# Optimization experiments

Hardware: AMD Instinct MI355X
Metric: run time of the kernel (lower is better)

## Reference

```python
import jax, jax.numpy as jnp
import numpy as np


def setup_inputs() -> dict:
    N, E, D = 50000, 800000, 64
    key = jax.random.key(0)
    ks = jax.random.split(key, 8)
    s = 1.0 / np.sqrt(2 * D)
    inp = {
        "node_emb": jax.random.normal(ks[0], (N, D), dtype=jnp.float32),
        "edge_index": jax.random.randint(ks[1], (2, E), 0, N, dtype=jnp.int64),
        "W1": jax.random.normal(ks[2], (2 * D, D), dtype=jnp.float32) * s,
        "b1": jnp.zeros((D,), dtype=jnp.float32),
        "W2": jax.random.normal(ks[3], (D, D), dtype=jnp.float32) * (1.0 / np.sqrt(D)),
        "b2": jnp.zeros((D,), dtype=jnp.float32),
        "Wg": jax.random.normal(ks[4], (D, D), dtype=jnp.float32) * (1.0 / np.sqrt(D)),
        "bg": jnp.zeros((D,), dtype=jnp.float32),
    }
    return inp


def reference(node_emb, edge_index, W1, b1, W2, b2, Wg, bg):
    # Gather pairwise embeddings along edges
    src, dst = edge_index[0], edge_index[1]
    pair_emb = jnp.concatenate([node_emb[src], node_emb[dst]], axis=-1)  # [E, 2D]
    # Interaction MLP (dropout in eval mode -> identity)
    h = jax.nn.relu(pair_emb @ W1 + b1)
    interaction = h @ W2 + b2  # [E, D]
    # Sigmoid gate
    gate = jax.nn.sigmoid(interaction @ Wg + bg)
    gated = interaction * gate  # [E, D]
    # Scatter-mean back to source nodes
    N = node_emb.shape[0]
    summed = jax.ops.segment_sum(gated, src, num_segments=N)  # [N, D]
    counts = jax.ops.segment_sum(jnp.ones((src.shape[0],), dtype=gated.dtype), src, num_segments=N)
    pooled = summed / jnp.maximum(counts, 1.0)[:, None]
    return pooled
```

## Files before the change

### kernel.cpp

```cpp
#include <hip/hip_runtime.h>


typedef unsigned short ushort_t;
typedef __attribute__((ext_vector_type(8))) short     bf16x8;
typedef __attribute__((ext_vector_type(8))) unsigned short u16x8;
typedef __attribute__((ext_vector_type(4))) float     f32x4;

constexpr int D        = 64;
constexpr int TILE     = 64;
constexpr int BLOCK    = 256;
constexpr int NFRAG    = 32;
constexpr int SLAB_B   = 4352;
constexpr int PAIR_STR = 136;
constexpr int H_STR    = 72;
constexpr float LOG2E  = 1.4426950408889634f;

static __device__ __forceinline__ ushort_t f2bf(float f) {
    union { float f; unsigned int u; } v; v.f = f;
    const unsigned int r = v.u + 0x7FFFu + ((v.u >> 16) & 1u);
    return (ushort_t)(r >> 16);
}

#if __has_builtin(__builtin_amdgcn_exp2f)
static __device__ __forceinline__ float fexp2(float x) { return __builtin_amdgcn_exp2f(x); }
#else
static __device__ __forceinline__ float fexp2(float x) {
    float r; asm("v_exp_f32 %0, %1" : "=v"(r) : "v"(x)); return r;
}
#endif
#if __has_builtin(__builtin_amdgcn_rcpf)
static __device__ __forceinline__ float frcp(float x) { return __builtin_amdgcn_rcpf(x); }
#else
static __device__ __forceinline__ float frcp(float x) {
    float r; asm("v_rcp_f32 %0, %1" : "=v"(r) : "v"(x)); return r;
}
#endif


__global__ void prep_kernel(const float* __restrict__ W1, const float* __restrict__ W2,
                            const float* __restrict__ Wg,
                            const float* __restrict__ b2, const float* __restrict__ bg,
                            const float* __restrict__ emb, const int* __restrict__ ei,
                            ushort_t* __restrict__ wpack, float* __restrict__ bgp,
                            ushort_t* __restrict__ emb_bf, int* __restrict__ cnt,
                            float* __restrict__ summed,
                            int total_emb, int cvt_blocks, int e4blocks, int E) {
    const int bid = blockIdx.x;
    if (bid < 64) {
        const int t = bid * 256 + threadIdx.x;
        const int f = t >> 9;
        const int l = (t >> 3) & 63;
        const int j = t & 7;
        const int k = ((f < 16) ? (f & 3) : ((f - 16) & 1)) * 32 + (l >> 4) * 8 + j;
        const int n = ((f < 16) ? (f >> 2) : (((f & 7)) >> 1)) * 16 + (l & 15);
        float v;
        if (f < 16)      v = W1[k * 64 + n];
        else if (f < 24) v = W2[k * 64 + n];
        else {
            float s = 0.f;
            const float* wr = W2 + k * 64;
#pragma unroll 8
            for (int m = 0; m < 64; ++m) s += wr[m] * Wg[m * 64 + n];
            v = s * LOG2E;
        }
        wpack[t] = f2bf(v);
    } else if (bid < 64 + cvt_blocks) {
        const int idx  = (bid - 64) * 256 + threadIdx.x;
        const int base = idx * 8;
        if (base < total_emb) {
            const float4 a = *(const float4*)(emb + base);
            const float4 b = *(const float4*)(emb + base + 4);
            u16x8 p;
            p[0]=f2bf(a.x); p[1]=f2bf(a.y); p[2]=f2bf(a.z); p[3]=f2bf(a.w);
            p[4]=f2bf(b.x); p[5]=f2bf(b.y); p[6]=f2bf(b.z); p[7]=f2bf(b.w);
            *(u16x8*)(emb_bf + base) = p;
        }
    } else if (bid == 64 + cvt_blocks) {
        const int n = threadIdx.x;
        if (n < 64) {
            float s = bg[n];
#pragma unroll 8
            for (int m = 0; m < 64; ++m) s += b2[m] * Wg[m * 64 + n];
            bgp[n] = s * LOG2E;
        }
    } else if (bid < 65 + cvt_blocks + e4blocks) {
        const int e = ((bid - 65 - cvt_blocks) * 256 + threadIdx.x) * 4;
        if (e + 3 < E) {
            const int4 v = *(const int4*)(ei + e);
            atomicAdd(&cnt[v.x], 1); atomicAdd(&cnt[v.y], 1);
            atomicAdd(&cnt[v.z], 1); atomicAdd(&cnt[v.w], 1);
        } else {
            for (int k = e; k < E; ++k) atomicAdd(&cnt[ei[k]], 1);
        }
    } else {
        const int idx  = (bid - 65 - cvt_blocks - e4blocks) * 256 + threadIdx.x;
        const int base = idx * 4;
        if (base < total_emb)
            *(float4*)(summed + base) = (float4){0.f, 0.f, 0.f, 0.f};
    }
}


__global__ void scan_block(const int* __restrict__ cnt, int* __restrict__ off,
                           int* __restrict__ bsum, int N) {
    __shared__ int s[256];
    const int t = threadIdx.x, i = blockIdx.x * 256 + t;
    const int x = (i < N) ? cnt[i] : 0;
    s[t] = x; __syncthreads();
    for (int d = 1; d < 256; d <<= 1) {
        const int v = (t >= d) ? s[t - d] : 0;
        __syncthreads();
        s[t] += v;
        __syncthreads();
    }
    if (i < N) off[i] = s[t] - x;
    if (t == 255) bsum[blockIdx.x] = s[255];
}

__global__ void scatter_idx(const int* __restrict__ ei, int* __restrict__ off,
                            const int* __restrict__ bsum, unsigned* __restrict__ sorted,
                            int E, int nb) {
    __shared__ int pref[256];
    const int t = threadIdx.x;
    const int x = (t < nb) ? bsum[t] : 0;
    pref[t] = x; __syncthreads();
    for (int d = 1; d < 256; d <<= 1) {
        const int v = (t >= d) ? pref[t - d] : 0;
        __syncthreads();
        pref[t] += v;
        __syncthreads();
    }
    const int e = (blockIdx.x * blockDim.x + t) * 4;
    if (e + 3 < E) {
        const int4 v = *(const int4*)(ei + e);
        const int4 d = *(const int4*)(ei + E + e);
        const int bx = v.x >> 8, by = v.y >> 8, bz = v.z >> 8, bw = v.w >> 8;
        sorted[(bx ? pref[bx - 1] : 0) + atomicAdd(&off[v.x], 1)] =
            ((unsigned)v.x << 16) | (unsigned)d.x;
        sorted[(by ? pref[by - 1] : 0) + atomicAdd(&off[v.y], 1)] =
            ((unsigned)v.y << 16) | (unsigned)d.y;
        sorted[(bz ? pref[bz - 1] : 0) + atomicAdd(&off[v.z], 1)] =
            ((unsigned)v.z << 16) | (unsigned)d.z;
        sorted[(bw ? pref[bw - 1] : 0) + atomicAdd(&off[v.w], 1)] =
            ((unsigned)v.w << 16) | (unsigned)d.w;
    } else {
        for (int k = e; k < E; ++k) {
            const int s = ei[k], b = s >> 8;
            sorted[(b ? pref[b - 1] : 0) + atomicAdd(&off[s], 1)] =
                ((unsigned)s << 16) | (unsigned)ei[E + k];
        }
    }
}


__global__ __launch_bounds__(BLOCK, 8)
void edge_mlp_mfma(const ushort_t* __restrict__ emb_bf,
                   const unsigned* __restrict__ sorted,
                   const ushort_t* __restrict__ wpack,
                   const float* __restrict__ b1, const float* __restrict__ b2,
                   const float* __restrict__ bgp,
                   const int*   __restrict__ cnt,
                   float* __restrict__ summed,
                   int E)
{
    __shared__ char  slab[4][SLAB_B];
    __shared__ int   srcIds[TILE];
    __shared__ float rcS[TILE];

    const int tid = threadIdx.x;

    {
        const int e = tid >> 2, q4 = tid & 3;
        ushort_t* prow = (ushort_t*)&slab[e >> 4][(e & 15) * (PAIR_STR * 2)];
        const int ide = blockIdx.x * TILE + e;
        if (ide < E) {
            const unsigned p = sorted[ide];
            const int s  = (int)(p >> 16);
            const int dn = (int)(p & 0xFFFFu);
            if (q4 == 0) { srcIds[e] = s; rcS[e] = frcp(fmaxf((float)cnt[s], 1.0f)); }
            const ushort_t* sr = emb_bf + (size_t)s  * D + q4 * 16;
            const ushort_t* dr = emb_bf + (size_t)dn * D + q4 * 16;
            *(u16x8*)&prow[q4 * 16]          = *(const u16x8*)sr;
            *(u16x8*)&prow[q4 * 16 + 8]      = *(const u16x8*)(sr + 8);
            *(u16x8*)&prow[64 + q4 * 16]     = *(const u16x8*)dr;
            *(u16x8*)&prow[64 + q4 * 16 + 8] = *(const u16x8*)(dr + 8);
        } else {
            if (q4 == 0) { srcIds[e] = -1; rcS[e] = 1.0f; }
            const u16x8 z = {0,0,0,0,0,0,0,0};
            *(u16x8*)&prow[q4 * 16]          = z;
            *(u16x8*)&prow[q4 * 16 + 8]      = z;
            *(u16x8*)&prow[64 + q4 * 16]     = z;
            *(u16x8*)&prow[64 + q4 * 16 + 8] = z;
        }
    }

    const int w    = tid >> 6;
    const int ln   = tid & 63;
    const int quad = ln >> 4;
    const int cn   = ln & 15;
    ushort_t* pairW = (ushort_t*)slab[w];
    ushort_t* hW    = (ushort_t*)slab[w];

    f32x4 acc1[4];
#pragma unroll
    for (int nt = 0; nt < 4; ++nt) {
        const float b = b1[nt * 16 + cn];
        acc1[nt] = (f32x4){b, b, b, b};
    }
#pragma unroll
    for (int kc = 0; kc < 4; ++kc) {
        const bf16x8 a = *(const bf16x8*)&pairW[cn * PAIR_STR + kc * 32 + quad * 8];
#pragma unroll
        for (int nt = 0; nt < 4; ++nt) {
            const bf16x8 bf = *(const bf16x8*)(wpack + ((nt * 4 + kc) * 64 + ln) * 8);
            acc1[nt] = __builtin_amdgcn_mfma_f32_16x16x32_bf16(a, bf, acc1[nt], 0, 0, 0);
        }
    }
#pragma unroll
    for (int nt = 0; nt < 4; ++nt)
#pragma unroll
        for (int r = 0; r < 4; ++r)
            hW[(quad * 4 + r) * H_STR + nt * 16 + cn] = f2bf(fmaxf(acc1[nt][r], 0.f));

    f32x4 acc2[4], accg[4];
#pragma unroll
    for (int nt = 0; nt < 4; ++nt) {
        const float b  = b2 [nt * 16 + cn];
        const float bG = bgp[nt * 16 + cn];
        acc2[nt] = (f32x4){b, b, b, b};
        accg[nt] = (f32x4){bG, bG, bG, bG};
    }
#pragma unroll
    for (int kc = 0; kc < 2; ++kc) {
        const bf16x8 a = *(const bf16x8*)&hW[cn * H_STR + kc * 32 + quad * 8];
#pragma unroll
        for (int nt = 0; nt < 4; ++nt) {
            const bf16x8 bf2 = *(const bf16x8*)(wpack + ((16 + nt * 2 + kc) * 64 + ln) * 8);
            const bf16x8 bfg = *(const bf16x8*)(wpack + ((24 + nt * 2 + kc) * 64 + ln) * 8);
            acc2[nt] = __builtin_amdgcn_mfma_f32_16x16x32_bf16(a, bf2, acc2[nt], 0, 0, 0);
            accg[nt] = __builtin_amdgcn_mfma_f32_16x16x32_bf16(a, bfg, accg[nt], 0, 0, 0);
        }
    }

    float P[4][4];
#pragma unroll
    for (int nt = 0; nt < 4; ++nt) {
#pragma unroll
        for (int r = 0; r < 4; ++r) {
            const float ex = fexp2(-accg[nt][r]);
            P[nt][r] = acc2[nt][r] * frcp(1.0f + ex);
        }
        P[nt][1] += P[nt][0];
        P[nt][2] += P[nt][1];
        P[nt][3] += P[nt][2];
    }

    {
        const int   rbase  = 16 * w;
        const int   myRow  = ln & 15;
        const int   mySrc  = srcIds[rbase + myRow];
        const float myRc   = rcS[rbase + myRow];
        const int   prevSrc = srcIds[rbase + ((myRow + 15) & 15)];
        unsigned bmask = ((unsigned)__ballot(mySrc != prevSrc) & 0xFFFFu) | 1u;
        const int q4r = 4 * quad;
        while (bmask) {
            const int a = __builtin_ctz(bmask);
            bmask &= (bmask - 1u);
            const int b = bmask ? __builtin_ctz(bmask) : 16;
            const int sseg = __builtin_amdgcn_readlane(mySrc, a);
            if (sseg >= 0) {
                const int lo  = a - q4r, hi = b - q4r;
                const int clo = lo < 0 ? 0 : (lo > 4 ? 4 : lo);
                const int chi = hi < 0 ? 0 : (hi > 4 ? 4 : hi);
                const bool ge1 = chi > 1, ge2 = chi > 2, ge3 = chi > 3;
                const bool l0 = clo > 0, l1 = clo > 1, l2 = clo > 2;
                const bool valid = chi > clo;
                float t[4];
#pragma unroll
                for (int nt = 0; nt < 4; ++nt) {
                    const float sh = ge2 ? (ge3 ? P[nt][3] : P[nt][2])
                                         : (ge1 ? P[nt][1] : P[nt][0]);
                    const float sl = l1 ? (l2 ? P[nt][2] : P[nt][1])
                                        : (l0 ? P[nt][0] : 0.f);
                    t[nt] = valid ? sh - sl : 0.f;
                }
                t[0] += __shfl_xor(t[0], 16); t[0] += __shfl_xor(t[0], 32);
                t[1] += __shfl_xor(t[1], 16); t[1] += __shfl_xor(t[1], 32);
                t[2] += __shfl_xor(t[2], 16); t[2] += __shfl_xor(t[2], 32);
                t[3] += __shfl_xor(t[3], 16); t[3] += __shfl_xor(t[3], 32);
                const float tot = (quad < 2) ? (quad == 0 ? t[0] : t[1])
                                             : (quad == 2 ? t[2] : t[3]);
                const float rc = __uint_as_float(
                    __builtin_amdgcn_readlane(__float_as_uint(myRc), a));
                unsafeAtomicAdd(&summed[(size_t)sseg * D + ln], tot * rc);
            }
        }
    }
}

extern "C" void kernel_launch(void* const* d_in, const int* in_sizes, int n_in,
                              void* d_out, int out_size, void* d_ws, size_t ws_size,
                              hipStream_t stream) {
    const float* node_emb   = (const float*)d_in[0];
    const int*   edge_index = (const int*)d_in[1];
    const float* W1 = (const float*)d_in[2];
    const float* b1 = (const float*)d_in[3];
    const float* W2 = (const float*)d_in[4];
    const float* b2 = (const float*)d_in[5];
    const float* Wg = (const float*)d_in[6];
    const float* bg = (const float*)d_in[7];

    const int N = in_sizes[0] / D;
    const int E = in_sizes[1] / 2;
    const int total_emb = N * D;

    int* cnt    = (int*)d_ws;
    int* off    = cnt + N;
    int* bsum   = off + N;
    unsigned* sorted = (unsigned*)(bsum + 256);
    float* bgp  = (float*)(sorted + E);
    ushort_t* wpack  = (ushort_t*)(bgp + 64);
    ushort_t* emb_bf = wpack + NFRAG * 512;

    float* summed = (float*)d_out;

    hipMemsetAsync(cnt, 0, sizeof(int) * (size_t)N, stream);

    const int cvt_blocks = (total_emb / 8 + 255) / 256;
    const int e4blocks   = ((E + 3) / 4 + 255) / 256;
    const int zblocks    = (total_emb / 4 + 255) / 256;
    prep_kernel<<<64 + cvt_blocks + 1 + e4blocks + zblocks, 256, 0, stream>>>(
        W1, W2, Wg, b2, bg, node_emb, edge_index,
        wpack, bgp, emb_bf, cnt, summed, total_emb, cvt_blocks, e4blocks, E);

    const int nblocks = (N + 255) / 256;
    scan_block <<<nblocks, 256, 0, stream>>>(cnt, off, bsum, N);
    scatter_idx<<<e4blocks, 256, 0, stream>>>(edge_index, off, bsum, sorted, E, nblocks);

    const int ntiles = (E + TILE - 1) / TILE;
    edge_mlp_mfma<<<ntiles, BLOCK, 0, stream>>>(emb_bf, sorted, wpack,
                                                b1, b2, bgp, cnt, summed, E);
}
```

Baseline: 237.5 us.

## Fuse preprocessing, count, scan and scatter into one cooperative kernel

Replaces the memset plus three preprocessing launches (prep, block scan, scatter) with a single cooperative persistent kernel that separates the phases with grid-wide syncs. Each block redoes the small block-sum scan locally in shared memory before scattering. The aim is to remove kernel launch gaps and the memset. The cost is a grid-stride loop over virtual blocks at limited occupancy, plus the overhead of the grid barriers. If the cooperative launch fails, it falls back to the old launches.

```diff
diff --git a/kernel.cpp b/kernel.cpp
--- a/kernel.cpp
+++ b/kernel.cpp
@@ -1,5 +1,8 @@
 #include <hip/hip_runtime.h>
-
+#include <hip/hip_cooperative_groups.h>
+
+
+namespace cg = cooperative_groups;
 
 typedef unsigned short ushort_t;
 typedef __attribute__((ext_vector_type(8))) short     bf16x8;
@@ -35,6 +38,133 @@
     float r; asm("v_rcp_f32 %0, %1" : "=v"(r) : "v"(x)); return r;
 }
 #endif
+
+
+struct AuxParams {
+    const float* W1; const float* W2; const float* Wg;
+    const float* b2; const float* bg;
+    const float* emb; const int* ei;
+    ushort_t* wpack; float* bgp; ushort_t* emb_bf;
+    int* cnt; int* off; int* bsum; unsigned* sorted; float* summed;
+    int N, E, total_emb, cvt_blocks, e4blocks, zblocks, nblocks;
+};
+
+__global__ __launch_bounds__(BLOCK, 8)
+void fused_aux(AuxParams P) {
+    cg::grid_group grid = cg::this_grid();
+    __shared__ int s[256];
+    const int tid = threadIdx.x;
+    const int G   = gridDim.x;
+
+    for (int i = blockIdx.x * BLOCK + tid; i < P.N; i += G * BLOCK) P.cnt[i] = 0;
+    grid.sync();
+
+    const int vb1 = 65 + P.cvt_blocks + P.e4blocks + P.zblocks;
+    for (int vb = blockIdx.x; vb < vb1; vb += G) {
+        if (vb < 64) {
+            const int t = vb * 256 + tid;
+            const int f = t >> 9;
+            const int l = (t >> 3) & 63;
+            const int j = t & 7;
+            const int k = ((f < 16) ? (f & 3) : ((f - 16) & 1)) * 32 + (l >> 4) * 8 + j;
+            const int n = ((f < 16) ? (f >> 2) : (((f & 7)) >> 1)) * 16 + (l & 15);
+            float v;
+            if (f < 16)      v = P.W1[k * 64 + n];
+            else if (f < 24) v = P.W2[k * 64 + n];
+            else {
+                float sacc = 0.f;
+                const float* wr = P.W2 + k * 64;
+#pragma unroll 8
+                for (int m = 0; m < 64; ++m) sacc += wr[m] * P.Wg[m * 64 + n];
+                v = sacc * LOG2E;
+            }
+            P.wpack[t] = f2bf(v);
+        } else if (vb < 64 + P.cvt_blocks) {
+            const int idx  = (vb - 64) * 256 + tid;
+            const int base = idx * 8;
+            if (base < P.total_emb) {
+                const float4 a = *(const float4*)(P.emb + base);
+                const float4 b = *(const float4*)(P.emb + base + 4);
+                u16x8 p;
+                p[0]=f2bf(a.x); p[1]=f2bf(a.y); p[2]=f2bf(a.z); p[3]=f2bf(a.w);
+                p[4]=f2bf(b.x); p[5]=f2bf(b.y); p[6]=f2bf(b.z); p[7]=f2bf(b.w);
+                *(u16x8*)(P.emb_bf + base) = p;
+            }
+        } else if (vb == 64 + P.cvt_blocks) {
+            const int n = tid;
+            if (n < 64) {
+                float sacc = P.bg[n];
+#pragma unroll 8
+                for (int m = 0; m < 64; ++m) sacc += P.b2[m] * P.Wg[m * 64 + n];
+                P.bgp[n] = sacc * LOG2E;
+            }
+        } else if (vb < 65 + P.cvt_blocks + P.e4blocks) {
+            const int e = ((vb - 65 - P.cvt_blocks) * 256 + tid) * 4;
+            if (e + 3 < P.E) {
+                const int4 v = *(const int4*)(P.ei + e);
+                atomicAdd(&P.cnt[v.x], 1); atomicAdd(&P.cnt[v.y], 1);
+                atomicAdd(&P.cnt[v.z], 1); atomicAdd(&P.cnt[v.w], 1);
+            } else {
+                for (int k = e; k < P.E; ++k) atomicAdd(&P.cnt[P.ei[k]], 1);
+            }
+        } else {
+            const int idx  = (vb - 65 - P.cvt_blocks - P.e4blocks) * 256 + tid;
+            const int base = idx * 4;
+            if (base < P.total_emb)
+                *(float4*)(P.summed + base) = (float4){0.f, 0.f, 0.f, 0.f};
+        }
+    }
+    grid.sync();
+
+    for (int vb = blockIdx.x; vb < P.nblocks; vb += G) {
+        const int i = vb * 256 + tid;
+        const int x = (i < P.N) ? P.cnt[i] : 0;
+        s[tid] = x; __syncthreads();
+        for (int d = 1; d < 256; d <<= 1) {
+            const int v = (tid >= d) ? s[tid - d] : 0;
+            __syncthreads();
+            s[tid] += v;
+            __syncthreads();
+        }
+        if (i < P.N) P.off[i] = s[tid] - x;
+        if (tid == 255) P.bsum[vb] = s[255];
+        __syncthreads();
+    }
+    grid.sync();
+
+    {
+        const int x = (tid < P.nblocks) ? P.bsum[tid] : 0;
+        s[tid] = x; __syncthreads();
+        for (int d = 1; d < 256; d <<= 1) {
+            const int v = (tid >= d) ? s[tid - d] : 0;
+            __syncthreads();
+            s[tid] += v;
+            __syncthreads();
+        }
+        for (int vb = blockIdx.x; vb < P.e4blocks; vb += G) {
+            const int e = (vb * 256 + tid) * 4;
+            if (e + 3 < P.E) {
+                const int4 v = *(const int4*)(P.ei + e);
+                const int4 d = *(const int4*)(P.ei + P.E + e);
+                const int bx = v.x >> 8, by = v.y >> 8, bz = v.z >> 8, bw = v.w >> 8;
+                P.sorted[(bx ? s[bx - 1] : 0) + atomicAdd(&P.off[v.x], 1)] =
+                    ((unsigned)v.x << 16) | (unsigned)d.x;
+                P.sorted[(by ? s[by - 1] : 0) + atomicAdd(&P.off[v.y], 1)] =
+                    ((unsigned)v.y << 16) | (unsigned)d.y;
+                P.sorted[(bz ? s[bz - 1] : 0) + atomicAdd(&P.off[v.z], 1)] =
+                    ((unsigned)v.z << 16) | (unsigned)d.z;
+                P.sorted[(bw ? s[bw - 1] : 0) + atomicAdd(&P.off[v.w], 1)] =
+                    ((unsigned)v.w << 16) | (unsigned)d.w;
+            } else {
+                for (int k = e; k < P.E; ++k) {
+                    const int sv = P.ei[k], b = sv >> 8;
+                    P.sorted[(b ? s[b - 1] : 0) + atomicAdd(&P.off[sv], 1)] =
+                        ((unsigned)sv << 16) | (unsigned)P.ei[P.E + k];
+                }
+            }
+        }
+    }
+}
 
 
 __global__ void prep_kernel(const float* __restrict__ W1, const float* __restrict__ W2,
@@ -100,7 +230,6 @@
     }
 }
 
-
 __global__ void scan_block(const int* __restrict__ cnt, int* __restrict__ off,
                            int* __restrict__ bsum, int N) {
     __shared__ int s[256];
@@ -324,18 +453,50 @@
 
     float* summed = (float*)d_out;
 
-    hipMemsetAsync(cnt, 0, sizeof(int) * (size_t)N, stream);
-
     const int cvt_blocks = (total_emb / 8 + 255) / 256;
     const int e4blocks   = ((E + 3) / 4 + 255) / 256;
     const int zblocks    = (total_emb / 4 + 255) / 256;
-    prep_kernel<<<64 + cvt_blocks + 1 + e4blocks + zblocks, 256, 0, stream>>>(
-        W1, W2, Wg, b2, bg, node_emb, edge_index,
-        wpack, bgp, emb_bf, cnt, summed, total_emb, cvt_blocks, e4blocks, E);
-
-    const int nblocks = (N + 255) / 256;
-    scan_block <<<nblocks, 256, 0, stream>>>(cnt, off, bsum, N);
-    scatter_idx<<<e4blocks, 256, 0, stream>>>(edge_index, off, bsum, sorted, E, nblocks);
+    const int nblocks    = (N + 255) / 256;
+
+    static int g_grid = -1;
+    if (g_grid < 0) {
+        int perCU = 0;
+        hipError_t oe = hipOccupancyMaxActiveBlocksPerMultiprocessor(
+            &perCU, reinterpret_cast<const void*>(&fused_aux), BLOCK, 0);
+        int nCU = 256;
+        hipDeviceProp_t prop;
+        int dev = 0;
+        if (hipGetDevice(&dev) == hipSuccess &&
+            hipGetDeviceProperties(&prop, dev) == hipSuccess)
+            nCU = prop.multiProcessorCount;
+        g_grid = (oe == hipSuccess && perCU > 0) ? perCU * nCU : 0;
+        if (g_grid > 4096) g_grid = 4096;
+    }
+
+    bool coop_ok = false;
+    if (g_grid > 0) {
+        AuxParams P;
+        P.W1 = W1; P.W2 = W2; P.Wg = Wg; P.b2 = b2; P.bg = bg;
+        P.emb = node_emb; P.ei = edge_index;
+        P.wpack = wpack; P.bgp = bgp; P.emb_bf = emb_bf;
+        P.cnt = cnt; P.off = off; P.bsum = bsum; P.sorted = sorted; P.summed = summed;
+        P.N = N; P.E = E; P.total_emb = total_emb;
+        P.cvt_blocks = cvt_blocks; P.e4blocks = e4blocks; P.zblocks = zblocks;
+        P.nblocks = nblocks;
+        void* kargs[] = { (void*)&P };
+        coop_ok = hipLaunchCooperativeKernel(reinterpret_cast<const void*>(&fused_aux),
+                                             dim3(g_grid), dim3(BLOCK), kargs, 0,
+                                             stream) == hipSuccess;
+    }
+
+    if (!coop_ok) {
+        hipMemsetAsync(cnt, 0, sizeof(int) * (size_t)N, stream);
+        prep_kernel<<<64 + cvt_blocks + 1 + e4blocks + zblocks, 256, 0, stream>>>(
+            W1, W2, Wg, b2, bg, node_emb, edge_index,
+            wpack, bgp, emb_bf, cnt, summed, total_emb, cvt_blocks, e4blocks, E);
+        scan_block <<<nblocks, 256, 0, stream>>>(cnt, off, bsum, N);
+        scatter_idx<<<e4blocks, 256, 0, stream>>>(edge_index, off, bsum, sorted, E, nblocks);
+    }
 
     const int ntiles = (E + TILE - 1) / TILE;
     edge_mlp_mfma<<<ntiles, BLOCK, 0, stream>>>(emb_bf, sorted, wpack,
```

After: 579.9 us. +144.2%, slower.

## Make edge MLP kernel persistent with double-buffered async LDS gathers

Applied to the files above, without the earlier changes.

Turns the edge MLP kernel into a persistent grid of 1280 blocks. Each block walks a contiguous range of 64-edge tiles and prefetches the next tile's source and destination embeddings straight into LDS with global_load_lds while the current tile's MFMAs run. Sorted indices, counts and biases are kept in registers, and the LDS layout is changed to match the MFMA fragment order, removing the padded slab and the shared srcIds/rcS arrays. The risks are fewer resident waves (launch bounds lowered to 5), hand-written vmcnt waits that must be exactly right, and segment boundaries that now cross tile edges in sequence within one block.

```diff
diff --git a/kernel.cpp b/kernel.cpp
--- a/kernel.cpp
+++ b/kernel.cpp
@@ -10,9 +10,7 @@
 constexpr int TILE     = 64;
 constexpr int BLOCK    = 256;
 constexpr int NFRAG    = 32;
-constexpr int SLAB_B   = 4352;
-constexpr int PAIR_STR = 136;
-constexpr int H_STR    = 72;
+constexpr int GRID_MLP = 1280;
 constexpr float LOG2E  = 1.4426950408889634f;
 
 static __device__ __forceinline__ ushort_t f2bf(float f) {
@@ -21,20 +19,31 @@
     return (ushort_t)(r >> 16);
 }
 
-#if __has_builtin(__builtin_amdgcn_exp2f)
-static __device__ __forceinline__ float fexp2(float x) { return __builtin_amdgcn_exp2f(x); }
-#else
 static __device__ __forceinline__ float fexp2(float x) {
     float r; asm("v_exp_f32 %0, %1" : "=v"(r) : "v"(x)); return r;
 }
-#endif
-#if __has_builtin(__builtin_amdgcn_rcpf)
-static __device__ __forceinline__ float frcp(float x) { return __builtin_amdgcn_rcpf(x); }
-#else
 static __device__ __forceinline__ float frcp(float x) {
     float r; asm("v_rcp_f32 %0, %1" : "=v"(r) : "v"(x)); return r;
 }
-#endif
+
+static __device__ __forceinline__ void gload16(const void* g, void* l) {
+    __builtin_amdgcn_global_load_lds(
+        (const __attribute__((address_space(1))) void*)g,
+        (__attribute__((address_space(3))) void*)l, 16, 0, 0);
+}
+
+static __device__ __forceinline__ void stage_tile(const ushort_t* __restrict__ emb_bf,
+                                                  char* lbuf, unsigned pk, bool valid,
+                                                  int cq) {
+    const unsigned s = valid ? (pk >> 16)     : 0u;
+    const unsigned d = valid ? (pk & 0xFFFFu) : 0u;
+    const ushort_t* sp = emb_bf + (size_t)s * D + cq * 8;
+    const ushort_t* dp = emb_bf + (size_t)d * D + cq * 8;
+    gload16(sp,      lbuf);
+    gload16(sp + 32, lbuf + 1024);
+    gload16(dp,      lbuf + 2048);
+    gload16(dp + 32, lbuf + 3072);
+}
 
 
 __global__ void prep_kernel(const float* __restrict__ W1, const float* __restrict__ W2,
@@ -153,7 +162,7 @@
 }
 
 
-__global__ __launch_bounds__(BLOCK, 8)
+__global__ __launch_bounds__(BLOCK, 5)
 void edge_mlp_mfma(const ushort_t* __restrict__ emb_bf,
                    const unsigned* __restrict__ sorted,
                    const ushort_t* __restrict__ wpack,
@@ -161,140 +170,158 @@
                    const float* __restrict__ bgp,
                    const int*   __restrict__ cnt,
                    float* __restrict__ summed,
-                   int E)
+                   int E, int ntiles, int nblk)
 {
-    __shared__ char  slab[4][SLAB_B];
-    __shared__ int   srcIds[TILE];
-    __shared__ float rcS[TILE];
-
-    const int tid = threadIdx.x;
-
-    {
-        const int e = tid >> 2, q4 = tid & 3;
-        ushort_t* prow = (ushort_t*)&slab[e >> 4][(e & 15) * (PAIR_STR * 2)];
-        const int ide = blockIdx.x * TILE + e;
-        if (ide < E) {
-            const unsigned p = sorted[ide];
-            const int s  = (int)(p >> 16);
-            const int dn = (int)(p & 0xFFFFu);
-            if (q4 == 0) { srcIds[e] = s; rcS[e] = frcp(fmaxf((float)cnt[s], 1.0f)); }
-            const ushort_t* sr = emb_bf + (size_t)s  * D + q4 * 16;
-            const ushort_t* dr = emb_bf + (size_t)dn * D + q4 * 16;
-            *(u16x8*)&prow[q4 * 16]          = *(const u16x8*)sr;
-            *(u16x8*)&prow[q4 * 16 + 8]      = *(const u16x8*)(sr + 8);
-            *(u16x8*)&prow[64 + q4 * 16]     = *(const u16x8*)dr;
-            *(u16x8*)&prow[64 + q4 * 16 + 8] = *(const u16x8*)(dr + 8);
-        } else {
-            if (q4 == 0) { srcIds[e] = -1; rcS[e] = 1.0f; }
-            const u16x8 z = {0,0,0,0,0,0,0,0};
-            *(u16x8*)&prow[q4 * 16]          = z;
-            *(u16x8*)&prow[q4 * 16 + 8]      = z;
-            *(u16x8*)&prow[64 + q4 * 16]     = z;
-            *(u16x8*)&prow[64 + q4 * 16 + 8] = z;
-        }
-    }
-
+    __shared__ __align__(16) char lds[4][2][4096];
+
+    const int tid  = threadIdx.x;
     const int w    = tid >> 6;
     const int ln   = tid & 63;
     const int quad = ln >> 4;
     const int cn   = ln & 15;
-    ushort_t* pairW = (ushort_t*)slab[w];
-    ushort_t* hW    = (ushort_t*)slab[w];
-
-    f32x4 acc1[4];
+    const int row  = ln & 15;
+
+    const int start = (int)(((long long)blockIdx.x * ntiles) / nblk);
+    const int end   = (int)(((long long)(blockIdx.x + 1) * ntiles) / nblk);
+    if (start >= end) return;
+
+    float bb1[4], bb2[4], bbg[4];
 #pragma unroll
     for (int nt = 0; nt < 4; ++nt) {
-        const float b = b1[nt * 16 + cn];
-        acc1[nt] = (f32x4){b, b, b, b};
-    }
-#pragma unroll
-    for (int kc = 0; kc < 4; ++kc) {
-        const bf16x8 a = *(const bf16x8*)&pairW[cn * PAIR_STR + kc * 32 + quad * 8];
+        bb1[nt] = b1 [nt * 16 + cn];
+        bb2[nt] = b2 [nt * 16 + cn];
+        bbg[nt] = bgp[nt * 16 + cn];
+    }
+
+    const int ebase = w * 16 + row;
+
+    unsigned pk_cur, pk_next;
+    bool     v_cur,  v_next;
+    int      cv_cur, cv_next = 0;
+    {
+        const int ide = start * TILE + ebase;
+        v_cur  = ide < E;
+        pk_cur = sorted[v_cur ? ide : (E - 1)];
+        stage_tile(emb_bf, lds[w][0], pk_cur, v_cur, quad);
+        cv_cur = cnt[v_cur ? (int)(pk_cur >> 16) : 0];
+        const int ide2 = (start + 1) * TILE + ebase;
+        v_next  = ide2 < E;
+        pk_next = sorted[v_next ? ide2 : (E - 1)];
+    }
+
+    int par = 0;
+    for (int t = start; t < end; ++t) {
+        char* cbuf = lds[w][par];
+
+        unsigned pk3 = 0; bool v3 = false;
+        if (t + 1 < end) {
+            stage_tile(emb_bf, lds[w][par ^ 1], pk_next, v_next, quad);
+            cv_next = cnt[v_next ? (int)(pk_next >> 16) : 0];
+            const int ide3 = (t + 2) * TILE + ebase;
+            v3  = ide3 < E;
+            pk3 = sorted[v3 ? ide3 : (E - 1)];
+            asm volatile("s_waitcnt vmcnt(6)" ::: "memory");
+        } else {
+            asm volatile("s_waitcnt vmcnt(0)" ::: "memory");
+        }
+
+        f32x4 acc1[4];
+#pragma unroll
+        for (int nt = 0; nt < 4; ++nt)
+            acc1[nt] = (f32x4){bb1[nt], bb1[nt], bb1[nt], bb1[nt]};
+#pragma unroll
+        for (int kc = 0; kc < 4; ++kc) {
+            const bf16x8 a = *(const bf16x8*)(cbuf + kc * 1024 + ln * 16);
+#pragma unroll
+            for (int nt = 0; nt < 4; ++nt) {
+                const bf16x8 bf = *(const bf16x8*)(wpack + ((nt * 4 + kc) * 64 + ln) * 8);
+                acc1[nt] = __builtin_amdgcn_mfma_f32_16x16x32_bf16(a, bf, acc1[nt], 0, 0, 0);
+            }
+        }
 #pragma unroll
         for (int nt = 0; nt < 4; ++nt) {
-            const bf16x8 bf = *(const bf16x8*)(wpack + ((nt * 4 + kc) * 64 + ln) * 8);
-            acc1[nt] = __builtin_amdgcn_mfma_f32_16x16x32_bf16(a, bf, acc1[nt], 0, 0, 0);
-        }
-    }
-#pragma unroll
-    for (int nt = 0; nt < 4; ++nt)
-#pragma unroll
-        for (int r = 0; r < 4; ++r)
-            hW[(quad * 4 + r) * H_STR + nt * 16 + cn] = f2bf(fmaxf(acc1[nt][r], 0.f));
-
-    f32x4 acc2[4], accg[4];
-#pragma unroll
-    for (int nt = 0; nt < 4; ++nt) {
-        const float b  = b2 [nt * 16 + cn];
-        const float bG = bgp[nt * 16 + cn];
-        acc2[nt] = (f32x4){b, b, b, b};
-        accg[nt] = (f32x4){bG, bG, bG, bG};
-    }
-#pragma unroll
-    for (int kc = 0; kc < 2; ++kc) {
-        const bf16x8 a = *(const bf16x8*)&hW[cn * H_STR + kc * 32 + quad * 8];
+            const int c = nt * 2 + (cn >> 3);
+            char* hb = cbuf + (c >> 2) * 1024 + (c & 3) * 256 + quad * 64 + (cn & 7) * 2;
+#pragma unroll
+            for (int rr = 0; rr < 4; ++rr)
+                *(ushort_t*)(hb + rr * 16) = f2bf(fmaxf(acc1[nt][rr], 0.f));
+        }
+
+        f32x4 acc2[4], accg[4];
 #pragma unroll
         for (int nt = 0; nt < 4; ++nt) {
-            const bf16x8 bf2 = *(const bf16x8*)(wpack + ((16 + nt * 2 + kc) * 64 + ln) * 8);
-            const bf16x8 bfg = *(const bf16x8*)(wpack + ((24 + nt * 2 + kc) * 64 + ln) * 8);
-            acc2[nt] = __builtin_amdgcn_mfma_f32_16x16x32_bf16(a, bf2, acc2[nt], 0, 0, 0);
-            accg[nt] = __builtin_amdgcn_mfma_f32_16x16x32_bf16(a, bfg, accg[nt], 0, 0, 0);
-        }
-    }
-
-    float P[4][4];
-#pragma unroll
-    for (int nt = 0; nt < 4; ++nt) {
-#pragma unroll
-        for (int r = 0; r < 4; ++r) {
-            const float ex = fexp2(-accg[nt][r]);
-            P[nt][r] = acc2[nt][r] * frcp(1.0f + ex);
-        }
-        P[nt][1] += P[nt][0];
-        P[nt][2] += P[nt][1];
-        P[nt][3] += P[nt][2];
-    }
-
-    {
-        const int   rbase  = 16 * w;
-        const int   myRow  = ln & 15;
-        const int   mySrc  = srcIds[rbase + myRow];
-        const float myRc   = rcS[rbase + myRow];
-        const int   prevSrc = srcIds[rbase + ((myRow + 15) & 15)];
-        unsigned bmask = ((unsigned)__ballot(mySrc != prevSrc) & 0xFFFFu) | 1u;
-        const int q4r = 4 * quad;
-        while (bmask) {
-            const int a = __builtin_ctz(bmask);
-            bmask &= (bmask - 1u);
-            const int b = bmask ? __builtin_ctz(bmask) : 16;
-            const int sseg = __builtin_amdgcn_readlane(mySrc, a);
-            if (sseg >= 0) {
-                const int lo  = a - q4r, hi = b - q4r;
-                const int clo = lo < 0 ? 0 : (lo > 4 ? 4 : lo);
-                const int chi = hi < 0 ? 0 : (hi > 4 ? 4 : hi);
-                const bool ge1 = chi > 1, ge2 = chi > 2, ge3 = chi > 3;
-                const bool l0 = clo > 0, l1 = clo > 1, l2 = clo > 2;
-                const bool valid = chi > clo;
-                float t[4];
-#pragma unroll
-                for (int nt = 0; nt < 4; ++nt) {
-                    const float sh = ge2 ? (ge3 ? P[nt][3] : P[nt][2])
-                                         : (ge1 ? P[nt][1] : P[nt][0]);
-                    const float sl = l1 ? (l2 ? P[nt][2] : P[nt][1])
-                                        : (l0 ? P[nt][0] : 0.f);
-                    t[nt] = valid ? sh - sl : 0.f;
+            acc2[nt] = (f32x4){bb2[nt], bb2[nt], bb2[nt], bb2[nt]};
+            accg[nt] = (f32x4){bbg[nt], bbg[nt], bbg[nt], bbg[nt]};
+        }
+#pragma unroll
+        for (int kc = 0; kc < 2; ++kc) {
+            const bf16x8 a = *(const bf16x8*)(cbuf + kc * 1024 + ln * 16);
+#pragma unroll
+            for (int nt = 0; nt < 4; ++nt) {
+                const bf16x8 bf2 = *(const bf16x8*)(wpack + ((16 + nt * 2 + kc) * 64 + ln) * 8);
+                const bf16x8 bfg = *(const bf16x8*)(wpack + ((24 + nt * 2 + kc) * 64 + ln) * 8);
+                acc2[nt] = __builtin_amdgcn_mfma_f32_16x16x32_bf16(a, bf2, acc2[nt], 0, 0, 0);
+                accg[nt] = __builtin_amdgcn_mfma_f32_16x16x32_bf16(a, bfg, accg[nt], 0, 0, 0);
+            }
+        }
+
+        float P[4][4];
+#pragma unroll
+        for (int nt = 0; nt < 4; ++nt) {
+#pragma unroll
+            for (int r = 0; r < 4; ++r) {
+                const float ex = fexp2(-accg[nt][r]);
+                P[nt][r] = acc2[nt][r] * frcp(1.0f + ex);
+            }
+            P[nt][1] += P[nt][0];
+            P[nt][2] += P[nt][1];
+            P[nt][3] += P[nt][2];
+        }
+
+        {
+            const int   mySrc = v_cur ? (int)(pk_cur >> 16) : -1;
+            const float myRc  = frcp(fmaxf((float)cv_cur, 1.0f));
+            const int   prevLane = (ln & 48) | ((ln + 15) & 15);
+            const int   prevSrc  = __shfl(mySrc, prevLane);
+            unsigned bmask = ((unsigned)__ballot(mySrc != prevSrc) & 0xFFFFu) | 1u;
+            const int q4r = 4 * quad;
+            while (bmask) {
+                const int a = __builtin_ctz(bmask);
+                bmask &= (bmask - 1u);
+                const int b = bmask ? __builtin_ctz(bmask) : 16;
+                const int sseg = __builtin_amdgcn_readlane(mySrc, a);
+                if (sseg >= 0) {
+                    const int lo  = a - q4r, hi = b - q4r;
+                    const int clo = lo < 0 ? 0 : (lo > 4 ? 4 : lo);
+                    const int chi = hi < 0 ? 0 : (hi > 4 ? 4 : hi);
+                    const bool ge1 = chi > 1, ge2 = chi > 2, ge3 = chi > 3;
+                    const bool l0 = clo > 0, l1 = clo > 1, l2 = clo > 2;
+                    const bool valid = chi > clo;
+                    float tt[4];
+#pragma unroll
+                    for (int nt = 0; nt < 4; ++nt) {
+                        const float sh = ge2 ? (ge3 ? P[nt][3] : P[nt][2])
+                                             : (ge1 ? P[nt][1] : P[nt][0]);
+                        const float sl = l1 ? (l2 ? P[nt][2] : P[nt][1])
+                                            : (l0 ? P[nt][0] : 0.f);
+                        tt[nt] = valid ? sh - sl : 0.f;
+                    }
+                    tt[0] += __shfl_xor(tt[0], 16); tt[0] += __shfl_xor(tt[0], 32);
+                    tt[1] += __shfl_xor(tt[1], 16); tt[1] += __shfl_xor(tt[1], 32);
+                    tt[2] += __shfl_xor(tt[2], 16); tt[2] += __shfl_xor(tt[2], 32);
+                    tt[3] += __shfl_xor(tt[3], 16); tt[3] += __shfl_xor(tt[3], 32);
+                    const float tot = (quad < 2) ? (quad == 0 ? tt[0] : tt[1])
+                                                 : (quad == 2 ? tt[2] : tt[3]);
+                    const float rc = __uint_as_float(
+                        __builtin_amdgcn_readlane(__float_as_uint(myRc), a));
+                    unsafeAtomicAdd(&summed[(size_t)sseg * D + ln], tot * rc);
                 }
-                t[0] += __shfl_xor(t[0], 16); t[0] += __shfl_xor(t[0], 32);
-                t[1] += __shfl_xor(t[1], 16); t[1] += __shfl_xor(t[1], 32);
-                t[2] += __shfl_xor(t[2], 16); t[2] += __shfl_xor(t[2], 32);
-                t[3] += __shfl_xor(t[3], 16); t[3] += __shfl_xor(t[3], 32);
-                const float tot = (quad < 2) ? (quad == 0 ? t[0] : t[1])
-                                             : (quad == 2 ? t[2] : t[3]);
-                const float rc = __uint_as_float(
-                    __builtin_amdgcn_readlane(__float_as_uint(myRc), a));
-                unsafeAtomicAdd(&summed[(size_t)sseg * D + ln], tot * rc);
             }
         }
+
+        pk_cur = pk_next; v_cur = v_next; cv_cur = cv_next;
+        pk_next = pk3;    v_next = v3;
+        par ^= 1;
     }
 }
 
@@ -338,6 +365,8 @@
     scatter_idx<<<e4blocks, 256, 0, stream>>>(edge_index, off, bsum, sorted, E, nblocks);
 
     const int ntiles = (E + TILE - 1) / TILE;
-    edge_mlp_mfma<<<ntiles, BLOCK, 0, stream>>>(emb_bf, sorted, wpack,
-                                                b1, b2, bgp, cnt, summed, E);
-}
+    const int nblk   = (ntiles < GRID_MLP) ? ntiles : GRID_MLP;
+    edge_mlp_mfma<<<nblk, BLOCK, 0, stream>>>(emb_bf, sorted, wpack,
+                                              b1, b2, bgp, cnt, summed,
+                                              E, ntiles, nblk);
+}
```

Result: slower. 453.5 us (+91.0%).
